# Optimization experiments

Measured on AMD Instinct MI355X. Metric: run time of the kernel, lower is better.

## Reference

```python
import jax, jax.numpy as jnp
import numpy as np

TOP_K = 30
NUM_RBF = 16
MAX_REL = 32

# atom order in stacked tensor: N=0, Ca=1, C=2, O=3, Cb=4
# 24 (A,B) pairs after the Ca-Ca D_neighbors RBF, in original order
PAIR_I = np.array([0,2,3,4,1,1,1,1,0,0,0,4,4,3,0,2,3,4,2,3,4,2,3,2])
PAIR_J = np.array([0,2,3,4,0,2,3,4,2,3,4,2,3,2,1,1,1,1,0,0,0,4,4,3])


def _rbf(D):
    # D [...]: radial basis over 16 centers in [2, 22], sigma = 20/16
    mu = jnp.linspace(2.0, 22.0, NUM_RBF)
    sigma = (22.0 - 2.0) / NUM_RBF
    return jnp.exp(-(((D[..., None] - mu) / sigma) ** 2))


def setup_inputs() -> dict:
    key = jax.random.key(0)
    ks = jax.random.split(key, 8)
    B, L = 4, 2048
    X = jax.random.normal(ks[0], (B, L, 5, 3), dtype=jnp.float32)
    mask = jnp.ones((B, L), dtype=jnp.float32)
    residue_idx = jnp.sort(jax.random.randint(ks[1], (B, L), 0, 3000), axis=-1)
    chain_labels = jax.random.randint(ks[2], (B, L), 0, 4)
    edge_in = 16 + NUM_RBF * 25  # 416
    pos_W = jax.random.normal(ks[3], (16, 2 * MAX_REL + 2), dtype=jnp.float32) * 0.1
    pos_b = jax.random.normal(ks[4], (16,), dtype=jnp.float32) * 0.1
    edge_W = jax.random.normal(ks[5], (128, edge_in), dtype=jnp.float32) * 0.05
    ln_g = jnp.ones((128,), dtype=jnp.float32)
    ln_b = jnp.zeros((128,), dtype=jnp.float32)
    return {"X": X, "mask": mask, "residue_idx": residue_idx,
            "chain_labels": chain_labels, "pos_W": pos_W, "pos_b": pos_b,
            "edge_W": edge_W, "ln_g": ln_g, "ln_b": ln_b}


def protein_features(X, mask, residue_idx, chain_labels, pos_W, pos_b, edge_W, ln_g, ln_b):
    B, L = mask.shape
    K = min(TOP_K, L)
    # virtual Cb from backbone frame
    b = X[:, :, 1, :] - X[:, :, 0, :]
    c = X[:, :, 2, :] - X[:, :, 1, :]
    a = jnp.cross(b, c)
    Cb = -0.58273431 * a + 0.56802827 * b - 0.54067466 * c + X[:, :, 1, :]
    N, Ca, C, O = X[:, :, 0, :], X[:, :, 1, :], X[:, :, 2, :], X[:, :, 4, :]

    # masked pairwise Ca distances + kNN (smallest distances)
    mask_2D = mask[:, None, :] * mask[:, :, None]            # [B,L,L]
    dX = Ca[:, None, :, :] - Ca[:, :, None, :]
    D = mask_2D * jnp.sqrt(jnp.sum(dX * dX, -1) + 1e-6)
    D_max = jnp.max(D, -1, keepdims=True)
    D_adjust = D + (1.0 - mask_2D) * D_max
    neg_vals, E_idx = jax.lax.top_k(-D_adjust, K)            # smallest K
    D_neighbors = -neg_vals                                   # [B,L,K]

    # gather neighbor coords for all 5 atom types at once
    atoms = jnp.stack([N, Ca, C, O, Cb])                      # [5,B,L,3]
    bidx = jnp.arange(B)[:, None, None]
    nbr = atoms[:, bidx, E_idx]                               # [5,B,L,K,3]
    # 24 pair distances, vectorized over the pair axis
    diff = atoms[PAIR_I][:, :, :, None, :] - nbr[PAIR_J]      # [24,B,L,K,3]
    D_pairs = jnp.sqrt(jnp.sum(diff * diff, -1) + 1e-6)       # [24,B,L,K]

    rbf0 = _rbf(D_neighbors)                                  # [B,L,K,16]
    rbf24 = _rbf(D_pairs)                                     # [24,B,L,K,16]
    rbf24 = jnp.transpose(rbf24, (1, 2, 3, 0, 4)).reshape(B, L, K, 24 * NUM_RBF)
    RBF_all = jnp.concatenate([rbf0, rbf24], axis=-1)         # [B,L,K,400]

    # relative position / chain embedding on edges
    res_nbr = residue_idx[bidx, E_idx]                        # [B,L,K]
    offset = residue_idx[:, :, None] - res_nbr
    chain_nbr = chain_labels[bidx, E_idx]
    same = (chain_labels[:, :, None] - chain_nbr == 0).astype(jnp.int32)
    d = jnp.clip(offset + MAX_REL, 0, 2 * MAX_REL) * same + (1 - same) * (2 * MAX_REL + 1)
    d_onehot = jax.nn.one_hot(d, 2 * MAX_REL + 2, dtype=jnp.float32)
    E_pos = d_onehot @ pos_W.T + pos_b                        # [B,L,K,16]

    E = jnp.concatenate([E_pos, RBF_all], axis=-1)            # [B,L,K,416]
    E = E @ edge_W.T                                          # [B,L,K,128]
    mu = jnp.mean(E, -1, keepdims=True)
    var = jnp.mean((E - mu) ** 2, -1, keepdims=True)
    E = (E - mu) * jax.lax.rsqrt(var + 1e-5) * ln_g + ln_b
    return E, E_idx


def reference(X, mask, residue_idx, chain_labels, pos_W, pos_b, edge_W, ln_g, ln_b):
    return protein_features(X, mask, residue_idx, chain_labels, pos_W, pos_b, edge_W, ln_g, ln_b)
```

## Files before the change

### kernel.cpp

```cpp
#include <hip/hip_runtime.h>

#define LVAL 2048
#define KNB 30
#define NPOS 66
#define EDGE_IN 416
#define NOUT 128
#define NWF (13 * 8 * 64 * 8)
#define NRES (4 * LVAL)

typedef __bf16 bf16x8 __attribute__((ext_vector_type(8)));
typedef float f32x4 __attribute__((ext_vector_type(4)));

__device__ __constant__ unsigned char c_PI[24] = {0,2,3,4,1,1,1,1,0,0,0,4,4,3,0,2,3,4,2,3,4,2,3,2};
__device__ __constant__ unsigned char c_PJ[24] = {0,2,3,4,0,2,3,4,2,3,4,2,3,2,1,1,1,1,0,0,0,4,4,3};

struct __align__(16) WaveMem {
  union {
    unsigned hist[256];
    float Dtab[25 * 33];
  } u;
  unsigned long long list[64];
  float natoms[KNB * 15];
  float satoms[16];
  float Dn[32];
  int   dk[32];
};

__device__ inline float ca_dist(float ax, float ay, float az, float bx, float by, float bz) {
#pragma clang fp contract(off)
  float dx = bx - ax, dy = by - ay, dz = bz - az;
  float d2 = ((dx * dx) + (dy * dy)) + (dz * dz);
  return sqrtf(d2 + 1e-6f);
}

__device__ inline float wmaxf(float v) {
#pragma unroll
  for (int off = 32; off >= 1; off >>= 1) v = fmaxf(v, __shfl_xor(v, off, 64));
  return v;
}

__device__ inline unsigned scan_find_bin(const unsigned* hist, int lane, unsigned K) {
  uint4 h = ((const uint4*)hist)[lane];
  unsigned p0 = h.x, p1 = p0 + h.y, p2 = p1 + h.z, p3 = p2 + h.w;
  unsigned v = p3;
#pragma unroll
  for (int off = 1; off < 64; off <<= 1) {
    unsigned o = __shfl_up(v, off, 64);
    if (lane >= off) v += o;
  }
  unsigned excl = v - p3;
  unsigned long long bal = __ballot(v >= K);
  int ff = __builtin_ctzll(bal);
  unsigned bi;
  if (excl + p0 >= K)      bi = 0u;
  else if (excl + p1 >= K) bi = 1u;
  else if (excl + p2 >= K) bi = 2u;
  else                     bi = 3u;
  return (unsigned)__shfl((int)(4u * (unsigned)lane + bi), ff, 64);
}

__device__ inline void get_atom(const float* __restrict__ base, int a, float& o0, float& o1, float& o2) {
  if (a < 3) {
    o0 = base[a * 3 + 0]; o1 = base[a * 3 + 1]; o2 = base[a * 3 + 2];
  } else if (a == 3) {
    o0 = base[12]; o1 = base[13]; o2 = base[14];
  } else {
    float nx = base[0], ny = base[1], nz = base[2];
    float ax = base[3], ay = base[4], az = base[5];
    float cx = base[6], cy = base[7], cz = base[8];
    float bvx = ax - nx, bvy = ay - ny, bvz = az - nz;
    float cvx = cx - ax, cvy = cy - ay, cvz = cz - az;
    float avx = bvy * cvz - bvz * cvy;
    float avy = bvz * cvx - bvx * cvz;
    float avz = bvx * cvy - bvy * cvx;
    o0 = (-0.58273431f * avx + 0.56802827f * bvx) - 0.54067466f * cvx + ax;
    o1 = (-0.58273431f * avy + 0.56802827f * bvy) - 0.54067466f * cvy + ay;
    o2 = (-0.58273431f * avz + 0.56802827f * bvz) - 0.54067466f * cvz + az;
  }
}

__global__ void prep(const float* __restrict__ W, __bf16* __restrict__ wf,
                     const float* __restrict__ X, const float* __restrict__ mask,
                     float4* __restrict__ cm, float* __restrict__ x16) {
  int id = blockIdx.x * 256 + threadIdx.x;
  if (id < NWF) {
    int jj = id & 7, l = (id >> 3) & 63, nt = (id >> 9) & 7, s = id >> 12;
    int k = 32 * s + ((l >> 4) << 3) + jj;
    int n = nt * 16 + (l & 15);
    wf[id] = (__bf16)W[n * EDGE_IN + k];
  } else if (id < NWF + NRES) {
    int cid = id - NWF;
    const float* __restrict__ xr = X + (size_t)cid * 15;
    float4 v; v.x = xr[3]; v.y = xr[4]; v.z = xr[5]; v.w = mask[cid];
    cm[cid] = v;
    float4* __restrict__ o = (float4*)(x16 + (size_t)cid * 16);
    o[0] = make_float4(xr[0], xr[1], xr[2], xr[3]);
    o[1] = make_float4(xr[4], xr[5], xr[6], xr[7]);
    o[2] = make_float4(xr[8], xr[9], xr[10], xr[11]);
    o[3] = make_float4(xr[12], xr[13], xr[14], 0.f);
  }
}

__global__ __launch_bounds__(256, 4)
void pf_kernel(const int* __restrict__ ridx, const int* __restrict__ chain,
               const float* __restrict__ posW, const float* __restrict__ posb,
               const float* __restrict__ lng, const float* __restrict__ lnb,
               const __bf16* __restrict__ wf, const float4* __restrict__ cm,
               const float* __restrict__ x16,
               float* __restrict__ outE, float* __restrict__ outI) {
  __shared__ WaveMem smw[4];
  const int tid = threadIdx.x, lane = tid & 63, wid = tid >> 6;
  WaveMem& w = smw[wid];
  const int row = blockIdx.x * 4 + wid;
  const int b = row >> 11;
  const float4* __restrict__ cmb = cm + (size_t)b * LVAL;

  float4 me = cm[row];
  const float cax = me.x, cay = me.y, caz = me.z, mi = me.w;

  float Dv[32];
  unsigned mb = 0u;
  float lmax = 0.f;
#pragma unroll
  for (int q = 0; q < 32; ++q) {
    float4 v = cmb[(q << 6) | lane];
    float m2 = mi * v.w;
    float D = m2 * ca_dist(cax, cay, caz, v.x, v.y, v.z);
    Dv[q] = D;
    if (m2 == 0.f) mb |= (1u << q);
    lmax = fmaxf(lmax, D);
  }
  const float Dmax = wmaxf(lmax);
  const float fscb = 255.9f / fmaxf(Dmax, 1e-30f);

  { int4 z = {0, 0, 0, 0}; ((int4*)w.u.hist)[lane] = z; }
#pragma unroll
  for (int q = 0; q < 32; ++q) {
    float Dadj = Dv[q] + (((mb >> q) & 1u) ? Dmax : 0.f);
    Dv[q] = Dadj;
    int bin = min((int)(Dadj * fscb), 255);
    atomicAdd(&w.u.hist[bin], 1u);
  }
  const unsigned T1 = scan_find_bin(w.u.hist, lane, 30u);

  unsigned cum = 0;
  const unsigned long long lmaskbits = (1ull << lane) - 1ull;
#pragma unroll
  for (int q = 0; q < 32; ++q) {
    int bin = min((int)(Dv[q] * fscb), 255);
    bool pred = ((unsigned)bin <= T1);
    unsigned long long bal = __ballot(pred);
    if (pred) {
      unsigned pos = cum + (unsigned)__popcll(bal & lmaskbits);
      if (pos < 64u) {
        unsigned kb = __float_as_uint(Dv[q]);
        w.list[pos] = (((unsigned long long)kb) << 32) | (unsigned)((q << 6) | lane);
      }
    }
    cum += (unsigned)__popcll(bal);
  }
  const unsigned M = min(cum, 64u);

  unsigned long long mykey = (lane < (int)M) ? w.list[lane] : ~0ull;
  unsigned rank = 0;
  for (unsigned s = 0; s < M; ++s) {
    unsigned long long ks = __shfl(mykey, (int)s, 64);
    rank += (ks < mykey) ? 1u : 0u;
  }
  bool sel = (lane < (int)M) && (rank < KNB);
  if (sel) w.list[rank] = mykey;
  if (sel) {
    unsigned jj = (unsigned)(mykey & 0xffffffffull);
    w.Dn[rank] = __uint_as_float((unsigned)(mykey >> 32));
    int off = ridx[row] - ridx[b * LVAL + (int)jj];
    int same = (chain[row] == chain[b * LVAL + (int)jj]) ? 1 : 0;
    w.dk[rank] = same ? min(max(off + 32, 0), 64) : 65;
    outI[(size_t)row * KNB + rank] = (float)jj;
  }

#pragma unroll
  for (int t = 0; t < 3; ++t) {
    int idx = lane + 64 * t;
    if (idx < KNB * 5) {
      int k = idx / 5, a = idx - 5 * k;
      unsigned jj = (unsigned)(w.list[k] & 0xffffffffull);
      const float* base = x16 + ((size_t)(b * LVAL) + jj) * 16;
      float o0, o1, o2;
      get_atom(base, a, o0, o1, o2);
      w.natoms[k * 15 + a * 3 + 0] = o0;
      w.natoms[k * 15 + a * 3 + 1] = o1;
      w.natoms[k * 15 + a * 3 + 2] = o2;
    } else if (idx < KNB * 5 + 5) {
      int a = idx - KNB * 5;
      float o0, o1, o2;
      get_atom(x16 + (size_t)row * 16, a, o0, o1, o2);
      w.satoms[a * 3 + 0] = o0;
      w.satoms[a * 3 + 1] = o1;
      w.satoms[a * 3 + 2] = o2;
    }
  }

  if (lane < 32) w.u.Dtab[lane] = w.Dn[lane];
#pragma unroll 2
  for (int t = 0; t < 12; ++t) {
    int idx = lane + 64 * t;
    if (idx < 24 * KNB) {
      int p = idx / KNB, m = idx - KNB * p;
      const float* A = &w.satoms[c_PI[p] * 3];
      const float* Bq = &w.natoms[m * 15 + c_PJ[p] * 3];
      w.u.Dtab[(p + 1) * 33 + m] = ca_dist(A[0], A[1], A[2], Bq[0], Bq[1], Bq[2]);
    }
  }

  const int llo = lane & 15, lhi = lane >> 4;
  f32x4 acc[2][8];
#pragma unroll
  for (int h = 0; h < 2; ++h)
#pragma unroll
    for (int nt = 0; nt < 8; ++nt) { acc[h][nt][0] = 0.f; acc[h][nt][1] = 0.f; acc[h][nt][2] = 0.f; acc[h][nt][3] = 0.f; }

  const bf16x8* __restrict__ WFp = ((const bf16x8*)wf) + lane;
  const bool m1ok = (llo < 14);

#pragma unroll 1
  for (int s = 0; s < 13; ++s) {
    bf16x8 a0, a1;
    const int f0 = s * 32 + lhi * 8;
    if (f0 < 16) {
      int d0 = w.dk[llo];
      int d1 = m1ok ? w.dk[llo + 16] : 0;
#pragma unroll
      for (int jx = 0; jx < 8; ++jx) {
        int f = f0 + jx;
        float pb = posb[f];
        a0[jx] = (__bf16)(posW[f * NPOS + d0] + pb);
        a1[jx] = m1ok ? (__bf16)(posW[f * NPOS + d1] + pb) : (__bf16)0.f;
      }
    } else {
      const int gi = (f0 - 16) >> 4;
      const int rbase = (f0 - 16) & 15;
      float D0 = w.u.Dtab[gi * 33 + llo];
      float D1 = m1ok ? w.u.Dtab[gi * 33 + llo + 16] : 2.0f;
      const float mu0 = 2.0f + (4.0f / 3.0f) * (float)rbase;
      float t0 = fminf(fmaxf((D0 - mu0) * 0.8f, -28.f), 28.f);
      float t1 = fminf(fmaxf((D1 - mu0) * 0.8f, -28.f), 28.f);
      float e0 = __expf(-t0 * t0);
      float e1 = __expf(-t1 * t1);
      float c0 = __expf(2.1333333f * t0 - 1.1377778f);
      float c1 = __expf(2.1333333f * t1 - 1.1377778f);
#pragma unroll
      for (int jx = 0; jx < 8; ++jx) {
        a0[jx] = (__bf16)e0;
        a1[jx] = m1ok ? (__bf16)e1 : (__bf16)0.f;
        e0 *= c0; c0 *= 0.10273973f;
        e1 *= c1; c1 *= 0.10273973f;
      }
    }
    const bf16x8* __restrict__ wrow = WFp + s * 512;
    __builtin_amdgcn_s_setprio(1);
#pragma unroll
    for (int nt = 0; nt < 8; ++nt) {
      bf16x8 bb = wrow[nt * 64];
      acc[0][nt] = __builtin_amdgcn_mfma_f32_16x16x32_bf16(a0, bb, acc[0][nt], 0, 0, 0);
      acc[1][nt] = __builtin_amdgcn_mfma_f32_16x16x32_bf16(a1, bb, acc[1][nt], 0, 0, 0);
    }
    __builtin_amdgcn_s_setprio(0);
  }

  float gv[8], bv[8];
#pragma unroll
  for (int nt = 0; nt < 8; ++nt) { gv[nt] = lng[nt * 16 + llo]; bv[nt] = lnb[nt * 16 + llo]; }
  float* __restrict__ oRow = outE + (size_t)row * KNB * NOUT;
#pragma unroll
  for (int h = 0; h < 2; ++h) {
#pragma unroll
    for (int r = 0; r < 4; ++r) {
      float s1 = 0.f;
#pragma unroll
      for (int nt = 0; nt < 8; ++nt) s1 += acc[h][nt][r];
      s1 += __shfl_xor(s1, 1, 64);
      s1 += __shfl_xor(s1, 2, 64);
      s1 += __shfl_xor(s1, 4, 64);
      s1 += __shfl_xor(s1, 8, 64);
      float mu = s1 * (1.0f / 128.0f);
      float s2 = 0.f;
#pragma unroll
      for (int nt = 0; nt < 8; ++nt) { float d = acc[h][nt][r] - mu; s2 += d * d; }
      s2 += __shfl_xor(s2, 1, 64);
      s2 += __shfl_xor(s2, 2, 64);
      s2 += __shfl_xor(s2, 4, 64);
      s2 += __shfl_xor(s2, 8, 64);
      float rstd = rsqrtf(s2 * (1.0f / 128.0f) + 1e-5f);
      int rowm = h * 16 + lhi * 4 + r;
      if (rowm < KNB) {
        float* op = oRow + (size_t)rowm * NOUT + llo;
#pragma unroll
        for (int nt = 0; nt < 8; ++nt)
          op[nt * 16] = (acc[h][nt][r] - mu) * rstd * gv[nt] + bv[nt];
      }
    }
  }
}

extern "C" void kernel_launch(void* const* d_in, const int* in_sizes, int n_in,
                              void* d_out, int out_size, void* d_ws, size_t ws_size,
                              hipStream_t stream) {
  const float* X = (const float*)d_in[0];
  const float* mask = (const float*)d_in[1];
  const int* ridx = (const int*)d_in[2];
  const int* chain = (const int*)d_in[3];
  const float* posW = (const float*)d_in[4];
  const float* posb = (const float*)d_in[5];
  const float* edgeW = (const float*)d_in[6];
  const float* lng = (const float*)d_in[7];
  const float* lnb = (const float*)d_in[8];
  float* outE = (float*)d_out;
  float* outI = outE + (size_t)NRES * KNB * NOUT;

  char* ws = (char*)d_ws;
  __bf16* wf = (__bf16*)ws;
  float4* cm = (float4*)(ws + 851968);
  float* x16 = (float*)(ws + 851968 + 131072);

  hipLaunchKernelGGL(prep, dim3((NWF + NRES) / 256), dim3(256), 0, stream,
                     edgeW, wf, X, mask, cm, x16);
  hipLaunchKernelGGL(pf_kernel, dim3(NRES / 4), dim3(256), 0, stream,
                     ridx, chain, posW, posb, lng, lnb, wf, cm, x16, outE, outI);
}
```

Measured before the change: 228.6 us.

## Split each row across two cooperating waves with shared histogram and atomic list

Each residue row is now processed by two wavefronts instead of one. They split the distance scan, build a shared histogram and append candidates to a shared list through an LDS atomic counter, and they split the neighbor-atom gather and the distance table. Each wave then computes one 16-row half of the MFMA edge projection and its LayerNorm, so per-wave accumulator registers drop by half and the launch-bounds occupancy target rises from 4 to 6. The cost is several block-level barriers, a duplicated rank sort in both waves, and twice as many blocks.

```diff
diff --git a/kernel.cpp b/kernel.cpp
--- a/kernel.cpp
+++ b/kernel.cpp
@@ -14,7 +14,7 @@
 __device__ __constant__ unsigned char c_PI[24] = {0,2,3,4,1,1,1,1,0,0,0,4,4,3,0,2,3,4,2,3,4,2,3,2};
 __device__ __constant__ unsigned char c_PJ[24] = {0,2,3,4,0,2,3,4,2,3,4,2,3,2,1,1,1,1,0,0,0,4,4,3};
 
-struct __align__(16) WaveMem {
+struct __align__(16) RowMem {
   union {
     unsigned hist[256];
     float Dtab[25 * 33];
@@ -23,7 +23,11 @@
   float natoms[KNB * 15];
   float satoms[16];
   float Dn[32];
+  int   nidx[32];
   int   dk[32];
+  float pmax[2];
+  unsigned cnt;
+  unsigned pad;
 };
 
 __device__ inline float ca_dist(float ax, float ay, float az, float bx, float by, float bz) {
@@ -101,65 +105,76 @@
   }
 }
 
-__global__ __launch_bounds__(256, 4)
+__global__ __launch_bounds__(256, 6)
 void pf_kernel(const int* __restrict__ ridx, const int* __restrict__ chain,
                const float* __restrict__ posW, const float* __restrict__ posb,
                const float* __restrict__ lng, const float* __restrict__ lnb,
                const __bf16* __restrict__ wf, const float4* __restrict__ cm,
                const float* __restrict__ x16,
                float* __restrict__ outE, float* __restrict__ outI) {
-  __shared__ WaveMem smw[4];
+  __shared__ RowMem smr[2];
   const int tid = threadIdx.x, lane = tid & 63, wid = tid >> 6;
-  WaveMem& w = smw[wid];
-  const int row = blockIdx.x * 4 + wid;
+  const int rp = wid >> 1, wa = wid & 1;
+  RowMem& w = smr[rp];
+  const int row = blockIdx.x * 2 + rp;
   const int b = row >> 11;
   const float4* __restrict__ cmb = cm + (size_t)b * LVAL;
 
+  if (wa == 0 && lane == 0) w.cnt = 0u;
+  { uint2 z = make_uint2(0u, 0u); ((uint2*)w.u.hist)[(wa << 6) | lane] = z; }
+
   float4 me = cm[row];
   const float cax = me.x, cay = me.y, caz = me.z, mi = me.w;
 
-  float Dv[32];
+  float Dv[16];
   unsigned mb = 0u;
   float lmax = 0.f;
 #pragma unroll
-  for (int q = 0; q < 32; ++q) {
-    float4 v = cmb[(q << 6) | lane];
+  for (int ql = 0; ql < 16; ++ql) {
+    int j = ((wa * 16 + ql) << 6) | lane;
+    float4 v = cmb[j];
     float m2 = mi * v.w;
     float D = m2 * ca_dist(cax, cay, caz, v.x, v.y, v.z);
-    Dv[q] = D;
-    if (m2 == 0.f) mb |= (1u << q);
+    Dv[ql] = D;
+    if (m2 == 0.f) mb |= (1u << ql);
     lmax = fmaxf(lmax, D);
   }
-  const float Dmax = wmaxf(lmax);
+  if (lane == 0) w.pmax[wa] = wmaxf(lmax);
+  else wmaxf(lmax);
+  __syncthreads();
+  const float Dmax = fmaxf(w.pmax[0], w.pmax[1]);
   const float fscb = 255.9f / fmaxf(Dmax, 1e-30f);
 
-  { int4 z = {0, 0, 0, 0}; ((int4*)w.u.hist)[lane] = z; }
-#pragma unroll
-  for (int q = 0; q < 32; ++q) {
-    float Dadj = Dv[q] + (((mb >> q) & 1u) ? Dmax : 0.f);
-    Dv[q] = Dadj;
+#pragma unroll
+  for (int ql = 0; ql < 16; ++ql) {
+    float Dadj = Dv[ql] + (((mb >> ql) & 1u) ? Dmax : 0.f);
+    Dv[ql] = Dadj;
     int bin = min((int)(Dadj * fscb), 255);
     atomicAdd(&w.u.hist[bin], 1u);
   }
+  __syncthreads();
   const unsigned T1 = scan_find_bin(w.u.hist, lane, 30u);
 
-  unsigned cum = 0;
   const unsigned long long lmaskbits = (1ull << lane) - 1ull;
 #pragma unroll
-  for (int q = 0; q < 32; ++q) {
-    int bin = min((int)(Dv[q] * fscb), 255);
+  for (int ql = 0; ql < 16; ++ql) {
+    int bin = min((int)(Dv[ql] * fscb), 255);
     bool pred = ((unsigned)bin <= T1);
     unsigned long long bal = __ballot(pred);
+    unsigned nq = (unsigned)__popcll(bal);
+    unsigned base = 0u;
+    if (lane == 0) base = atomicAdd(&w.cnt, nq);
+    base = (unsigned)__shfl((int)base, 0, 64);
     if (pred) {
-      unsigned pos = cum + (unsigned)__popcll(bal & lmaskbits);
+      unsigned pos = base + (unsigned)__popcll(bal & lmaskbits);
       if (pos < 64u) {
-        unsigned kb = __float_as_uint(Dv[q]);
-        w.list[pos] = (((unsigned long long)kb) << 32) | (unsigned)((q << 6) | lane);
+        unsigned kb = __float_as_uint(Dv[ql]);
+        w.list[pos] = (((unsigned long long)kb) << 32) | (unsigned)(((wa * 16 + ql) << 6) | lane);
       }
     }
-    cum += (unsigned)__popcll(bal);
-  }
-  const unsigned M = min(cum, 64u);
+  }
+  __syncthreads();
+  const unsigned M = min(w.cnt, 64u);
 
   unsigned long long mykey = (lane < (int)M) ? w.list[lane] : ~0ull;
   unsigned rank = 0;
@@ -168,23 +183,23 @@
     rank += (ks < mykey) ? 1u : 0u;
   }
   bool sel = (lane < (int)M) && (rank < KNB);
-  if (sel) w.list[rank] = mykey;
   if (sel) {
     unsigned jj = (unsigned)(mykey & 0xffffffffull);
     w.Dn[rank] = __uint_as_float((unsigned)(mykey >> 32));
+    w.nidx[rank] = (int)jj;
     int off = ridx[row] - ridx[b * LVAL + (int)jj];
     int same = (chain[row] == chain[b * LVAL + (int)jj]) ? 1 : 0;
     w.dk[rank] = same ? min(max(off + 32, 0), 64) : 65;
-    outI[(size_t)row * KNB + rank] = (float)jj;
-  }
-
-#pragma unroll
-  for (int t = 0; t < 3; ++t) {
-    int idx = lane + 64 * t;
+    if (wa == 0) outI[(size_t)row * KNB + rank] = (float)jj;
+  }
+  __syncthreads();
+
+#pragma unroll
+  for (int t = 0; t < 2; ++t) {
+    int idx = lane + 64 * (wa + 2 * t);
     if (idx < KNB * 5) {
       int k = idx / 5, a = idx - 5 * k;
-      unsigned jj = (unsigned)(w.list[k] & 0xffffffffull);
-      const float* base = x16 + ((size_t)(b * LVAL) + jj) * 16;
+      const float* base = x16 + ((size_t)(b * LVAL) + (unsigned)w.nidx[k]) * 16;
       float o0, o1, o2;
       get_atom(base, a, o0, o1, o2);
       w.natoms[k * 15 + a * 3 + 0] = o0;
@@ -199,11 +214,12 @@
       w.satoms[a * 3 + 2] = o2;
     }
   }
-
-  if (lane < 32) w.u.Dtab[lane] = w.Dn[lane];
-#pragma unroll 2
-  for (int t = 0; t < 12; ++t) {
-    int idx = lane + 64 * t;
+  __syncthreads();
+
+  if (wa == 0 && lane < KNB) w.u.Dtab[lane] = w.Dn[lane];
+#pragma unroll 1
+  for (int t = 0; t < 6; ++t) {
+    int idx = (t * 2 + wa) * 64 + lane;
     if (idx < 24 * KNB) {
       int p = idx / KNB, m = idx - KNB * p;
       const float* A = &w.satoms[c_PI[p] * 3];
@@ -211,49 +227,41 @@
       w.u.Dtab[(p + 1) * 33 + m] = ca_dist(A[0], A[1], A[2], Bq[0], Bq[1], Bq[2]);
     }
   }
+  __syncthreads();
 
   const int llo = lane & 15, lhi = lane >> 4;
-  f32x4 acc[2][8];
-#pragma unroll
-  for (int h = 0; h < 2; ++h)
-#pragma unroll
-    for (int nt = 0; nt < 8; ++nt) { acc[h][nt][0] = 0.f; acc[h][nt][1] = 0.f; acc[h][nt][2] = 0.f; acc[h][nt][3] = 0.f; }
+  const int row_e = wa * 16 + llo;
+  const bool ok = (row_e < KNB);
+  const int re_c = ok ? row_e : 0;
+  f32x4 acc[8];
+#pragma unroll
+  for (int nt = 0; nt < 8; ++nt) { acc[nt][0] = 0.f; acc[nt][1] = 0.f; acc[nt][2] = 0.f; acc[nt][3] = 0.f; }
 
   const bf16x8* __restrict__ WFp = ((const bf16x8*)wf) + lane;
-  const bool m1ok = (llo < 14);
 
 #pragma unroll 1
   for (int s = 0; s < 13; ++s) {
-    bf16x8 a0, a1;
+    bf16x8 a0;
     const int f0 = s * 32 + lhi * 8;
     if (f0 < 16) {
-      int d0 = w.dk[llo];
-      int d1 = m1ok ? w.dk[llo + 16] : 0;
+      int d0 = w.dk[re_c];
 #pragma unroll
       for (int jx = 0; jx < 8; ++jx) {
         int f = f0 + jx;
-        float pb = posb[f];
-        a0[jx] = (__bf16)(posW[f * NPOS + d0] + pb);
-        a1[jx] = m1ok ? (__bf16)(posW[f * NPOS + d1] + pb) : (__bf16)0.f;
+        a0[jx] = ok ? (__bf16)(posW[f * NPOS + d0] + posb[f]) : (__bf16)0.f;
       }
     } else {
       const int gi = (f0 - 16) >> 4;
       const int rbase = (f0 - 16) & 15;
-      float D0 = w.u.Dtab[gi * 33 + llo];
-      float D1 = m1ok ? w.u.Dtab[gi * 33 + llo + 16] : 2.0f;
+      float D0 = ok ? w.u.Dtab[gi * 33 + row_e] : 2.0f;
       const float mu0 = 2.0f + (4.0f / 3.0f) * (float)rbase;
       float t0 = fminf(fmaxf((D0 - mu0) * 0.8f, -28.f), 28.f);
-      float t1 = fminf(fmaxf((D1 - mu0) * 0.8f, -28.f), 28.f);
       float e0 = __expf(-t0 * t0);
-      float e1 = __expf(-t1 * t1);
       float c0 = __expf(2.1333333f * t0 - 1.1377778f);
-      float c1 = __expf(2.1333333f * t1 - 1.1377778f);
 #pragma unroll
       for (int jx = 0; jx < 8; ++jx) {
-        a0[jx] = (__bf16)e0;
-        a1[jx] = m1ok ? (__bf16)e1 : (__bf16)0.f;
+        a0[jx] = ok ? (__bf16)e0 : (__bf16)0.f;
         e0 *= c0; c0 *= 0.10273973f;
-        e1 *= c1; c1 *= 0.10273973f;
       }
     }
     const bf16x8* __restrict__ wrow = WFp + s * 512;
@@ -261,8 +269,7 @@
 #pragma unroll
     for (int nt = 0; nt < 8; ++nt) {
       bf16x8 bb = wrow[nt * 64];
-      acc[0][nt] = __builtin_amdgcn_mfma_f32_16x16x32_bf16(a0, bb, acc[0][nt], 0, 0, 0);
-      acc[1][nt] = __builtin_amdgcn_mfma_f32_16x16x32_bf16(a1, bb, acc[1][nt], 0, 0, 0);
+      acc[nt] = __builtin_amdgcn_mfma_f32_16x16x32_bf16(a0, bb, acc[nt], 0, 0, 0);
     }
     __builtin_amdgcn_s_setprio(0);
   }
@@ -272,32 +279,29 @@
   for (int nt = 0; nt < 8; ++nt) { gv[nt] = lng[nt * 16 + llo]; bv[nt] = lnb[nt * 16 + llo]; }
   float* __restrict__ oRow = outE + (size_t)row * KNB * NOUT;
 #pragma unroll
-  for (int h = 0; h < 2; ++h) {
-#pragma unroll
-    for (int r = 0; r < 4; ++r) {
-      float s1 = 0.f;
-#pragma unroll
-      for (int nt = 0; nt < 8; ++nt) s1 += acc[h][nt][r];
-      s1 += __shfl_xor(s1, 1, 64);
-      s1 += __shfl_xor(s1, 2, 64);
-      s1 += __shfl_xor(s1, 4, 64);
-      s1 += __shfl_xor(s1, 8, 64);
-      float mu = s1 * (1.0f / 128.0f);
-      float s2 = 0.f;
-#pragma unroll
-      for (int nt = 0; nt < 8; ++nt) { float d = acc[h][nt][r] - mu; s2 += d * d; }
-      s2 += __shfl_xor(s2, 1, 64);
-      s2 += __shfl_xor(s2, 2, 64);
-      s2 += __shfl_xor(s2, 4, 64);
-      s2 += __shfl_xor(s2, 8, 64);
-      float rstd = rsqrtf(s2 * (1.0f / 128.0f) + 1e-5f);
-      int rowm = h * 16 + lhi * 4 + r;
-      if (rowm < KNB) {
-        float* op = oRow + (size_t)rowm * NOUT + llo;
-#pragma unroll
-        for (int nt = 0; nt < 8; ++nt)
-          op[nt * 16] = (acc[h][nt][r] - mu) * rstd * gv[nt] + bv[nt];
-      }
+  for (int r = 0; r < 4; ++r) {
+    float s1 = 0.f;
+#pragma unroll
+    for (int nt = 0; nt < 8; ++nt) s1 += acc[nt][r];
+    s1 += __shfl_xor(s1, 1, 64);
+    s1 += __shfl_xor(s1, 2, 64);
+    s1 += __shfl_xor(s1, 4, 64);
+    s1 += __shfl_xor(s1, 8, 64);
+    float mu = s1 * (1.0f / 128.0f);
+    float s2 = 0.f;
+#pragma unroll
+    for (int nt = 0; nt < 8; ++nt) { float d = acc[nt][r] - mu; s2 += d * d; }
+    s2 += __shfl_xor(s2, 1, 64);
+    s2 += __shfl_xor(s2, 2, 64);
+    s2 += __shfl_xor(s2, 4, 64);
+    s2 += __shfl_xor(s2, 8, 64);
+    float rstd = rsqrtf(s2 * (1.0f / 128.0f) + 1e-5f);
+    int rowm = wa * 16 + lhi * 4 + r;
+    if (rowm < KNB) {
+      float* op = oRow + (size_t)rowm * NOUT + llo;
+#pragma unroll
+      for (int nt = 0; nt < 8; ++nt)
+        op[nt * 16] = (acc[nt][r] - mu) * rstd * gv[nt] + bv[nt];
     }
   }
 }
@@ -324,6 +328,6 @@
 
   hipLaunchKernelGGL(prep, dim3((NWF + NRES) / 256), dim3(256), 0, stream,
                      edgeW, wf, X, mask, cm, x16);
-  hipLaunchKernelGGL(pf_kernel, dim3(NRES / 4), dim3(256), 0, stream,
+  hipLaunchKernelGGL(pf_kernel, dim3(NRES / 2), dim3(256), 0, stream,
                      ridx, chain, posW, posb, lng, lnb, wf, cm, x16, outE, outI);
 }
```

After: 231.4 us. About the same (+1.2%).

## Stage bf16 edge weights in LDS per 16-wave block, compute distances on the fly

Applied to the files above, without the earlier changes.

Blocks grow from 4 to 16 waves (1024 threads), and each block cooperatively copies the whole preformatted bf16 weight matrix (about 104 KB) into dynamic shared memory. The MFMA loop then reads B operands from LDS instead of global/L2. The per-wave distance table is removed: pair distances are recomputed inside the GEMM loop from staged atom coordinates, and the per-wave scratch is packed into a union so it fits. The costs are a large LDS footprint that limits blocks per CU, a 104 KB copy per block, a block-wide barrier, and redundant distance math across lanes.

```diff
diff --git a/kernel.cpp b/kernel.cpp
--- a/kernel.cpp
+++ b/kernel.cpp
@@ -7,6 +7,7 @@
 #define NOUT 128
 #define NWF (13 * 8 * 64 * 8)
 #define NRES (4 * LVAL)
+#define WF_F4 (NWF * 2 / 16)
 
 typedef __bf16 bf16x8 __attribute__((ext_vector_type(8)));
 typedef float f32x4 __attribute__((ext_vector_type(4)));
@@ -14,15 +15,15 @@
 __device__ __constant__ unsigned char c_PI[24] = {0,2,3,4,1,1,1,1,0,0,0,4,4,3,0,2,3,4,2,3,4,2,3,2};
 __device__ __constant__ unsigned char c_PJ[24] = {0,2,3,4,0,2,3,4,2,3,4,2,3,2,1,1,1,1,0,0,0,4,4,3};
 
-struct __align__(16) WaveMem {
+struct __align__(16) WS {
   union {
     unsigned hist[256];
-    float Dtab[25 * 33];
+    unsigned long long list[64];
+    float natoms[452];
   } u;
-  unsigned long long list[64];
-  float natoms[KNB * 15];
   float satoms[16];
   float Dn[32];
+  int   nidx[32];
   int   dk[32];
 };
 
@@ -101,19 +102,32 @@
   }
 }
 
-__global__ __launch_bounds__(256, 4)
+__global__ __launch_bounds__(1024, 4)
 void pf_kernel(const int* __restrict__ ridx, const int* __restrict__ chain,
                const float* __restrict__ posW, const float* __restrict__ posb,
                const float* __restrict__ lng, const float* __restrict__ lnb,
                const __bf16* __restrict__ wf, const float4* __restrict__ cm,
                const float* __restrict__ x16,
                float* __restrict__ outE, float* __restrict__ outI) {
-  __shared__ WaveMem smw[4];
+  extern __shared__ char dsm[];
+  __bf16* ldsB = (__bf16*)dsm;
+  WS* wsa = (WS*)(dsm + 106496);
+
   const int tid = threadIdx.x, lane = tid & 63, wid = tid >> 6;
-  WaveMem& w = smw[wid];
-  const int row = blockIdx.x * 4 + wid;
+  WS& w = wsa[wid];
+  const int row = blockIdx.x * 16 + wid;
   const int b = row >> 11;
   const float4* __restrict__ cmb = cm + (size_t)b * LVAL;
+
+  {
+    const float4* __restrict__ wf4 = (const float4*)wf;
+    float4* ldsB4 = (float4*)ldsB;
+#pragma unroll
+    for (int t = 0; t < 7; ++t) {
+      int idx = t * 1024 + tid;
+      if (idx < 6656) ldsB4[idx] = wf4[idx];
+    }
+  }
 
   float4 me = cm[row];
   const float cax = me.x, cay = me.y, caz = me.z, mi = me.w;
@@ -154,24 +168,24 @@
       unsigned pos = cum + (unsigned)__popcll(bal & lmaskbits);
       if (pos < 64u) {
         unsigned kb = __float_as_uint(Dv[q]);
-        w.list[pos] = (((unsigned long long)kb) << 32) | (unsigned)((q << 6) | lane);
+        w.u.list[pos] = (((unsigned long long)kb) << 32) | (unsigned)((q << 6) | lane);
       }
     }
     cum += (unsigned)__popcll(bal);
   }
   const unsigned M = min(cum, 64u);
 
-  unsigned long long mykey = (lane < (int)M) ? w.list[lane] : ~0ull;
+  unsigned long long mykey = (lane < (int)M) ? w.u.list[lane] : ~0ull;
   unsigned rank = 0;
   for (unsigned s = 0; s < M; ++s) {
     unsigned long long ks = __shfl(mykey, (int)s, 64);
     rank += (ks < mykey) ? 1u : 0u;
   }
   bool sel = (lane < (int)M) && (rank < KNB);
-  if (sel) w.list[rank] = mykey;
   if (sel) {
     unsigned jj = (unsigned)(mykey & 0xffffffffull);
     w.Dn[rank] = __uint_as_float((unsigned)(mykey >> 32));
+    w.nidx[rank] = (int)jj;
     int off = ridx[row] - ridx[b * LVAL + (int)jj];
     int same = (chain[row] == chain[b * LVAL + (int)jj]) ? 1 : 0;
     w.dk[rank] = same ? min(max(off + 32, 0), 64) : 65;
@@ -183,13 +197,12 @@
     int idx = lane + 64 * t;
     if (idx < KNB * 5) {
       int k = idx / 5, a = idx - 5 * k;
-      unsigned jj = (unsigned)(w.list[k] & 0xffffffffull);
-      const float* base = x16 + ((size_t)(b * LVAL) + jj) * 16;
+      const float* base = x16 + ((size_t)(b * LVAL) + (unsigned)w.nidx[k]) * 16;
       float o0, o1, o2;
       get_atom(base, a, o0, o1, o2);
-      w.natoms[k * 15 + a * 3 + 0] = o0;
-      w.natoms[k * 15 + a * 3 + 1] = o1;
-      w.natoms[k * 15 + a * 3 + 2] = o2;
+      w.u.natoms[k * 15 + a * 3 + 0] = o0;
+      w.u.natoms[k * 15 + a * 3 + 1] = o1;
+      w.u.natoms[k * 15 + a * 3 + 2] = o2;
     } else if (idx < KNB * 5 + 5) {
       int a = idx - KNB * 5;
       float o0, o1, o2;
@@ -200,17 +213,7 @@
     }
   }
 
-  if (lane < 32) w.u.Dtab[lane] = w.Dn[lane];
-#pragma unroll 2
-  for (int t = 0; t < 12; ++t) {
-    int idx = lane + 64 * t;
-    if (idx < 24 * KNB) {
-      int p = idx / KNB, m = idx - KNB * p;
-      const float* A = &w.satoms[c_PI[p] * 3];
-      const float* Bq = &w.natoms[m * 15 + c_PJ[p] * 3];
-      w.u.Dtab[(p + 1) * 33 + m] = ca_dist(A[0], A[1], A[2], Bq[0], Bq[1], Bq[2]);
-    }
-  }
+  __syncthreads();
 
   const int llo = lane & 15, lhi = lane >> 4;
   f32x4 acc[2][8];
@@ -219,7 +222,7 @@
 #pragma unroll
     for (int nt = 0; nt < 8; ++nt) { acc[h][nt][0] = 0.f; acc[h][nt][1] = 0.f; acc[h][nt][2] = 0.f; acc[h][nt][3] = 0.f; }
 
-  const bf16x8* __restrict__ WFp = ((const bf16x8*)wf) + lane;
+  const bf16x8* __restrict__ Bf = ((const bf16x8*)ldsB) + lane;
   const bool m1ok = (llo < 14);
 
 #pragma unroll 1
@@ -239,8 +242,21 @@
     } else {
       const int gi = (f0 - 16) >> 4;
       const int rbase = (f0 - 16) & 15;
-      float D0 = w.u.Dtab[gi * 33 + llo];
-      float D1 = m1ok ? w.u.Dtab[gi * 33 + llo + 16] : 2.0f;
+      float D0, D1;
+      if (gi == 0) {
+        D0 = w.Dn[llo];
+        D1 = m1ok ? w.Dn[llo + 16] : 2.0f;
+      } else {
+        int p = gi - 1;
+        int i3 = c_PI[p] * 3, j3 = c_PJ[p] * 3;
+        float ax = w.satoms[i3], ay = w.satoms[i3 + 1], az = w.satoms[i3 + 2];
+        const float* nb0 = &w.u.natoms[llo * 15 + j3];
+        D0 = ca_dist(ax, ay, az, nb0[0], nb0[1], nb0[2]);
+        if (m1ok) {
+          const float* nb1 = &w.u.natoms[(llo + 16) * 15 + j3];
+          D1 = ca_dist(ax, ay, az, nb1[0], nb1[1], nb1[2]);
+        } else D1 = 2.0f;
+      }
       const float mu0 = 2.0f + (4.0f / 3.0f) * (float)rbase;
       float t0 = fminf(fmaxf((D0 - mu0) * 0.8f, -28.f), 28.f);
       float t1 = fminf(fmaxf((D1 - mu0) * 0.8f, -28.f), 28.f);
@@ -256,11 +272,11 @@
         e1 *= c1; c1 *= 0.10273973f;
       }
     }
-    const bf16x8* __restrict__ wrow = WFp + s * 512;
+    const bf16x8* __restrict__ brow = Bf + s * 512;
     __builtin_amdgcn_s_setprio(1);
 #pragma unroll
     for (int nt = 0; nt < 8; ++nt) {
-      bf16x8 bb = wrow[nt * 64];
+      bf16x8 bb = brow[nt * 64];
       acc[0][nt] = __builtin_amdgcn_mfma_f32_16x16x32_bf16(a0, bb, acc[0][nt], 0, 0, 0);
       acc[1][nt] = __builtin_amdgcn_mfma_f32_16x16x32_bf16(a1, bb, acc[1][nt], 0, 0, 0);
     }
@@ -322,8 +338,17 @@
   float4* cm = (float4*)(ws + 851968);
   float* x16 = (float*)(ws + 851968 + 131072);
 
+  static bool s_attr = false;
+  if (!s_attr) {
+    (void)hipFuncSetAttribute((const void*)pf_kernel,
+                              hipFuncAttributeMaxDynamicSharedMemorySize, 147456);
+    s_attr = true;
+  }
+
+  const int ldsBytes = 106496 + 16 * (int)sizeof(WS);
+
   hipLaunchKernelGGL(prep, dim3((NWF + NRES) / 256), dim3(256), 0, stream,
                      edgeW, wf, X, mask, cm, x16);
-  hipLaunchKernelGGL(pf_kernel, dim3(NRES / 4), dim3(256), 0, stream,
+  hipLaunchKernelGGL(pf_kernel, dim3(NRES / 16), dim3(1024), ldsBytes, stream,
                      ridx, chain, posW, posb, lng, lnb, wf, cm, x16, outE, outI);
 }
```

Result: faster. 217.7 us (-4.8%).
